# Kernel tuning notes

Hardware: AMD Instinct MI355X
Metric: run time of the kernel (lower is better)

The kernel has to match this reference:

```python
import jax, jax.numpy as jnp
import numpy as np

GAMMA = 0.9865
B, S, D = 8, 2048, 128


def setup_inputs() -> dict:
    key = jax.random.key(0)
    kq, kk, kv, kw = jax.random.split(key, 4)
    xq = jax.random.normal(kq, (B, S, D), dtype=jnp.float32)
    xk = jax.random.normal(kk, (B, S, D), dtype=jnp.float32)
    xv = jax.random.normal(kv, (B, S, D), dtype=jnp.float32)
    # NOTE: the original builds three Dense layers by repeating the SAME object,
    # so Q/K/V share a single no-bias weight matrix W.
    W = jax.random.normal(kw, (D, D), dtype=jnp.float32) * (1.0 / np.sqrt(D))
    return {"xq": xq, "xk": xk, "xv": xv, "W": W}


def _decay_matrix(seq_len, gamma):
    # Original: factors[i,j] = gamma^(i-j); keep upper triangle (j>=i); transpose.
    # Result: Dm[n,m] = gamma^(m-n) for n >= m, else 0 (lower triangular).
    n = jnp.arange(seq_len, dtype=jnp.float32)
    expo = n[None, :] - n[:, None]            # [S,S], entry (n,m) = m - n
    Dm = jnp.tril(jnp.float32(gamma) ** expo)  # zero out m > n before they'd matter
    return Dm


def reference(xq, xk, xv, W):
    Q = xq @ W
    K = xk @ W
    V = xv @ W
    d = Q.shape[-1]
    scores = jnp.einsum('bnd,bmd->bnm', Q, K) / jnp.sqrt(jnp.float32(d))
    Dm = _decay_matrix(Q.shape[1], GAMMA)
    # D /= reduce_sum(D, axis=1) ** 0.5  -> row-sums broadcast over LAST axis,
    # i.e. column m of D is divided by sqrt(rowsum[m]). Faithful to tf broadcasting.
    Dm = Dm / jnp.sqrt(jnp.sum(Dm, axis=1))
    scores = scores * Dm
    # per-batch norm: xs[n,m] / max(|sum_k xs[m,k]|, 1)  (tf broadcasting over last axis)
    s = jnp.sum(scores, axis=2)                       # [B,S]
    scores = scores / jnp.maximum(jnp.abs(s), 1.0)[:, None, :]
    return scores @ V
```

## Files before the change

kernel.cpp:

```cpp
#include <hip/hip_runtime.h>
#include <math.h>


constexpr int B = 8, S = 2048, D = 128;
constexpr int C = 64, NC = S / C;
constexpr int BS = B * S;
constexpr int NCH = B * NC;
#define GAMMA_F 0.9865f

typedef __attribute__((ext_vector_type(8))) short short8;
typedef __attribute__((ext_vector_type(8))) unsigned short ushort8;
typedef __attribute__((ext_vector_type(4))) float f32x4;

__device__ inline unsigned short f2bf(float f) {
  unsigned u = __builtin_bit_cast(unsigned, f);
  return (unsigned short)((u + 0x7FFF + ((u >> 16) & 1)) >> 16);
}
__device__ inline float bf2f(unsigned short h) {
  return __builtin_bit_cast(float, (unsigned)h << 16);
}

__global__ __launch_bounds__(128) void k_y(const float* __restrict__ xk,
                                           float* __restrict__ yc) {
  __shared__ float ksl[64];
  int bc = blockIdx.x, tid = threadIdx.x;
  float lgf = logf(GAMMA_F);
  if (tid < 64) {
    int n = (bc * 64 + tid) & (S - 1);
    float rs = (expf(-lgf * (float)(n + 1)) - 1.f) * (GAMMA_F / (1.f - GAMMA_F));
    ksl[tid] = expf(lgf * (float)n) / sqrtf(rs);
  }
  __syncthreads();
  const float* x = xk + (size_t)bc * 64 * 128 + tid;
  float a = 0.f;
#pragma unroll
  for (int j = 0; j < 64; j++) a = fmaf(ksl[j], x[j * 128], a);
  yc[(size_t)bc * 128 + tid] = a;
}

__global__ __launch_bounds__(512) void k_big(
    const float* __restrict__ xq, const float* __restrict__ xk,
    const float* __restrict__ xv, const float* __restrict__ W,
    const float* __restrict__ yc, unsigned short* __restrict__ qb,
    unsigned short* __restrict__ al, unsigned short* __restrict__ vbT,
    unsigned short* __restrict__ Hc) {
  __shared__ unsigned short qkv[3][64][136];
  __shared__ alignas(16) char ovl[36864];
  __shared__ float csp[128];
  __shared__ float ysum[128];
  __shared__ float cspp[4][128];
  __shared__ float invl[64];
  __shared__ float rsum_l[2][64];
  auto wt = (unsigned short(*)[136])ovl;
  auto kT = (unsigned short(*)[72])ovl;
  auto vT = (unsigned short(*)[72])(ovl + 18432);

  int bc = blockIdx.x, b = bc >> 5, c = bc & 31;
  int tid = threadIdx.x, w = tid >> 6, lane = tid & 63;
  int l15 = lane & 15, kg = (lane >> 4) * 8;
  float lgf = logf(GAMMA_F);

  for (int idx = tid; idx < 128 * 128; idx += 512) {
    int cc = idx >> 7, k = idx & 127;
    wt[cc][k] = f2bf(W[k * 128 + cc]);
  }
  if (tid < 128) {
    float a = 0.f;
    for (int cc = 0; cc < c; cc++) a += yc[(size_t)(b * NC + cc) * 128 + tid];
    ysum[tid] = a;
  }
  __syncthreads();

  int rt = w & 3, chh = w >> 2;
  {
    int arow = rt * 16 + l15;
    size_t grow = (size_t)(bc * 64 + arow) * 128;
    for (int mat = 0; mat < 3; mat++) {
      const float* X = (mat == 0) ? xq : ((mat == 1) ? xk : xv);
      f32x4 acc[4];
#pragma unroll
      for (int j = 0; j < 4; j++) acc[j] = (f32x4){0.f, 0.f, 0.f, 0.f};
#pragma unroll
      for (int t = 0; t < 4; t++) {
        int k0 = t * 32 + kg;
        const float* ap = X + grow + k0;
        float a8[8];
        *(f32x4*)(a8) = *(const f32x4*)ap;
        *(f32x4*)(a8 + 4) = *(const f32x4*)(ap + 4);
        short8 af;
#pragma unroll
        for (int i = 0; i < 8; i++) af[i] = (short)f2bf(a8[i]);
#pragma unroll
        for (int j = 0; j < 4; j++) {
          short8 bf = *(const short8*)&wt[(chh * 4 + j) * 16 + l15][k0];
          acc[j] = __builtin_amdgcn_mfma_f32_16x16x32_bf16(af, bf, acc[j], 0, 0, 0);
        }
      }
      int crow = rt * 16 + (lane >> 4) * 4;
#pragma unroll
      for (int rr = 0; rr < 4; rr++) {
        int row = crow + rr;
        int n = (bc * 64 + row) & (S - 1);
        float sc;
        if (mat == 0) {
          sc = expf(-lgf * (float)n) * 0.088388347f;
        } else if (mat == 1) {
          float rs = (expf(-lgf * (float)(n + 1)) - 1.f) * (GAMMA_F / (1.f - GAMMA_F));
          sc = expf(lgf * (float)n) / sqrtf(rs);
        } else {
          sc = 1.f;
        }
#pragma unroll
        for (int j = 0; j < 4; j++)
          qkv[mat][row][(chh * 4 + j) * 16 + l15] = f2bf(acc[j][rr] * sc);
      }
    }
  }
  {
    int d = tid & 127, q = tid >> 7;
    float part = 0.f;
#pragma unroll
    for (int k = 0; k < 32; k++) part = fmaf(ysum[32 * q + k], bf2f(wt[d][32 * q + k]), part);
    cspp[q][d] = part;
  }
  __syncthreads();

  if (tid < 128) csp[tid] = cspp[0][tid] + cspp[1][tid] + cspp[2][tid] + cspp[3][tid];
  {
    int row = tid >> 3, col = (tid & 7) * 16;
    unsigned short* dst = qb + (size_t)(bc * 64 + row) * 128 + col;
    *(ushort8*)dst = *(const ushort8*)&qkv[0][row][col];
    *(ushort8*)(dst + 8) = *(const ushort8*)&qkv[0][row][col + 8];
  }
  {
    int rt2 = w & 3, mh = w >> 2;
    int arow = rt2 * 16 + l15;
    int crow = rt2 * 16 + (lane >> 4) * 4;
    f32x4 a1[2];
#pragma unroll
    for (int mi = 0; mi < 2; mi++) a1[mi] = (f32x4){0.f, 0.f, 0.f, 0.f};
#pragma unroll
    for (int t = 0; t < 4; t++) {
      int k0 = t * 32 + kg;
      short8 af = *(const short8*)&qkv[0][arow][k0];
#pragma unroll
      for (int mi = 0; mi < 2; mi++) {
        short8 bf = *(const short8*)&qkv[1][(mh * 2 + mi) * 16 + l15][k0];
        a1[mi] = __builtin_amdgcn_mfma_f32_16x16x32_bf16(af, bf, a1[mi], 0, 0, 0);
      }
    }
    unsigned short* alg = al + (size_t)bc * 64 * 64;
    float rsp[4] = {0.f, 0.f, 0.f, 0.f};
#pragma unroll
    for (int mi = 0; mi < 2; mi++)
#pragma unroll
      for (int rr = 0; rr < 4; rr++) {
        int n_l = crow + rr, m_l = (mh * 2 + mi) * 16 + l15;
        float mv = (n_l >= m_l) ? a1[mi][rr] : 0.f;
        alg[n_l * 64 + m_l] = f2bf(mv);
        rsp[rr] += mv;
      }
#pragma unroll
    for (int rr = 0; rr < 4; rr++) {
      float r = rsp[rr];
      r += __shfl_xor(r, 1); r += __shfl_xor(r, 2);
      r += __shfl_xor(r, 4); r += __shfl_xor(r, 8);
      if (l15 == 0) rsum_l[mh][crow + rr] = r;
    }
  }
  {
    int d = tid & 127, mh2 = tid >> 7;
#pragma unroll
    for (int mg = 0; mg < 2; mg++) {
      ushort8 pk;
#pragma unroll
      for (int i = 0; i < 8; i++) pk[i] = qkv[1][mh2 * 16 + mg * 8 + i][d];
      *(ushort8*)&kT[d][mh2 * 16 + mg * 8] = pk;
    }
  }
  {
    int d = tid & 127, mh2 = tid >> 7;
#pragma unroll
    for (int mg = 0; mg < 2; mg++) {
      ushort8 pk;
#pragma unroll
      for (int i = 0; i < 8; i++) pk[i] = qkv[2][mh2 * 16 + mg * 8 + i][d];
      *(ushort8*)&vT[d][mh2 * 16 + mg * 8] = pk;
    }
  }
  __syncthreads();

  {
    int row = tid >> 3, part = tid & 7;
    ushort8 q8a = *(const ushort8*)&qkv[0][row][part * 16];
    ushort8 q8b = *(const ushort8*)&qkv[0][row][part * 16 + 8];
    float dot = 0.f;
#pragma unroll
    for (int ii = 0; ii < 8; ii++) {
      dot = fmaf(bf2f(q8a[ii]), csp[part * 16 + ii], dot);
      dot = fmaf(bf2f(q8b[ii]), csp[part * 16 + 8 + ii], dot);
    }
    dot += __shfl_xor(dot, 1); dot += __shfl_xor(dot, 2); dot += __shfl_xor(dot, 4);
    if (part == 0) {
      float s = rsum_l[0][row] + rsum_l[1][row] + dot;
      invl[row] = 1.f / fmaxf(fabsf(s), 1.f);
    }
  }
  __syncthreads();

  {
    int d = tid >> 2, ms = (tid & 3) * 16;
#pragma unroll
    for (int g = 0; g < 2; g++) {
      ushort8 v8 = *(const ushort8*)&vT[d][ms + g * 8];
      ushort8 o;
#pragma unroll
      for (int ii = 0; ii < 8; ii++) o[ii] = f2bf(bf2f(v8[ii]) * invl[ms + g * 8 + ii]);
      *(ushort8*)&vT[d][ms + g * 8] = o;
    }
  }
  __syncthreads();

  {
    f32x4 hacc[8];
#pragma unroll
    for (int j = 0; j < 8; j++) hacc[j] = (f32x4){0.f, 0.f, 0.f, 0.f};
#pragma unroll
    for (int t = 0; t < 2; t++) {
      int k0 = t * 32 + kg;
      short8 a2 = *(const short8*)&vT[w * 16 + l15][k0];
#pragma unroll
      for (int j = 0; j < 8; j++) {
        short8 bf = *(const short8*)&kT[j * 16 + l15][k0];
        hacc[j] = __builtin_amdgcn_mfma_f32_16x16x32_bf16(a2, bf, hacc[j], 0, 0, 0);
      }
    }
    unsigned short* g = Hc + (size_t)bc * D * D;
#pragma unroll
    for (int j = 0; j < 8; j++)
#pragma unroll
      for (int rr = 0; rr < 4; rr++)
        g[(size_t)(w * 16 + (lane >> 4) * 4 + rr) * D + j * 16 + l15] =
            f2bf(hacc[j][rr]);
  }
  {
    int d = tid >> 2, pp = (tid & 3) * 16;
    unsigned short* dst = vbT + (size_t)bc * D * C + (size_t)d * C + pp;
    *(ushort8*)(dst) = *(const ushort8*)&vT[d][pp];
    *(ushort8*)(dst + 8) = *(const ushort8*)&vT[d][pp + 8];
  }
}

__global__ __launch_bounds__(64) void k_gscan(const unsigned short* __restrict__ Hc,
                                              unsigned short* __restrict__ HS) {
  int b = blockIdx.x, gy = blockIdx.y, t = threadIdx.x;
  int d2 = gy * 4 + (t >> 4), d1 = (t & 15) * 8;
  size_t off = ((size_t)(b * NC) * D + d2) * D + d1;
  ushort8 v[NC];
#pragma unroll
  for (int c = 0; c < NC; c++)
    v[c] = *(const ushort8*)(Hc + off + (size_t)c * D * D);
  float run[8];
#pragma unroll
  for (int j = 0; j < 8; j++) run[j] = 0.f;
#pragma unroll
  for (int c = 0; c < NC; c++) {
    ushort8 o;
#pragma unroll
    for (int j = 0; j < 8; j++) {
      o[j] = f2bf(run[j]);
      run[j] += bf2f(v[c][j]);
    }
    *(ushort8*)(HS + off + (size_t)c * D * D) = o;
  }
}

__global__ __launch_bounds__(512) void k_out(
    const unsigned short* __restrict__ qb, const unsigned short* __restrict__ al,
    const unsigned short* __restrict__ vbT, const unsigned short* __restrict__ HS,
    float* __restrict__ out) {
  int bc = blockIdx.x, tid = threadIdx.x, w = tid >> 6, lane = tid & 63;
  int l15 = lane & 15;
  size_t base = (size_t)bc * C * D;
  int kg = (lane >> 4) * 8;
  int rt = w >> 1, ch = w & 1;
  int arow = rt * 16 + l15;
  int crow = rt * 16 + (lane >> 4) * 4;

  f32x4 acc[4];
#pragma unroll
  for (int j = 0; j < 4; j++) acc[j] = (f32x4){0.f, 0.f, 0.f, 0.f};
  const unsigned short* hrow = HS + (size_t)bc * D * D;
#pragma unroll
  for (int t = 0; t < 4; t++) {
    int k0 = t * 32 + kg;
    short8 af = *(const short8*)(qb + base + (size_t)arow * D + k0);
#pragma unroll
    for (int jj = 0; jj < 4; jj++) {
      int j = ch * 4 + jj;
      short8 bf = *(const short8*)(hrow + (size_t)(j * 16 + l15) * D + k0);
      acc[jj] = __builtin_amdgcn_mfma_f32_16x16x32_bf16(af, bf, acc[jj], 0, 0, 0);
    }
  }
  const unsigned short* alg = al + (size_t)bc * 64 * 64;
  const unsigned short* vt = vbT + (size_t)bc * D * C;
#pragma unroll
  for (int t = 0; t < 2; t++) {
    int k0 = t * 32 + kg;
    short8 af = *(const short8*)(alg + (size_t)arow * 64 + k0);
#pragma unroll
    for (int jj = 0; jj < 4; jj++) {
      int j = ch * 4 + jj;
      short8 bf = *(const short8*)(vt + (size_t)(j * 16 + l15) * C + k0);
      acc[jj] = __builtin_amdgcn_mfma_f32_16x16x32_bf16(af, bf, acc[jj], 0, 0, 0);
    }
  }
#pragma unroll
  for (int jj = 0; jj < 4; jj++)
#pragma unroll
    for (int rr = 0; rr < 4; rr++)
      out[base + (size_t)(crow + rr) * D + (ch * 4 + jj) * 16 + l15] = acc[jj][rr];
}

extern "C" void kernel_launch(void* const* d_in, const int* in_sizes, int n_in,
                              void* d_out, int out_size, void* d_ws, size_t ws_size,
                              hipStream_t stream) {
  const float* xq = (const float*)d_in[0];
  const float* xk = (const float*)d_in[1];
  const float* xv = (const float*)d_in[2];
  const float* W  = (const float*)d_in[3];
  float* out = (float*)d_out;

  char* p = (char*)d_ws;
  float* yc = (float*)p;                     p += (size_t)NCH * D * 4;
  unsigned short* qb  = (unsigned short*)p;  p += (size_t)BS * D * 2;
  unsigned short* al  = (unsigned short*)p;  p += (size_t)NCH * C * C * 2;
  unsigned short* vbT = (unsigned short*)p;  p += (size_t)NCH * D * C * 2;
  unsigned short* Hc  = (unsigned short*)p;  p += (size_t)NCH * D * D * 2;
  unsigned short* HS  = (unsigned short*)p;  p += (size_t)NCH * D * D * 2;

  hipLaunchKernelGGL(k_y, dim3(NCH), dim3(128), 0, stream, xk, yc);
  hipLaunchKernelGGL(k_big, dim3(NCH), dim3(512), 0, stream,
                     xq, xk, xv, W, yc, qb, al, vbT, Hc);
  hipLaunchKernelGGL(k_gscan, dim3(B, 32), dim3(64), 0, stream, Hc, HS);
  hipLaunchKernelGGL(k_out, dim3(NCH), dim3(512), 0, stream, qb, al, vbT, HS, out);
}
```

Baseline: 51.78 us.

## Fuse chunk-state prefix scan into output kernel and widen blocks to 1024 threads

Removes the separate k_gscan prefix-sum kernel and HS buffer. Each output block now sums the preceding chunks' Hc states itself into shared memory before the MFMA output step. k_big and the new output kernel are also redistributed to 1024 threads (16 waves), with work per wave halved. This saves a launch and a full HS write/read, but makes the per-block prefix sum redundant, so later chunks read up to 31 state matrices and the work is imbalanced across blocks.

```diff
diff --git a/kernel.cpp b/kernel.cpp
--- a/kernel.cpp
+++ b/kernel.cpp
@@ -38,7 +38,7 @@
   yc[(size_t)bc * 128 + tid] = a;
 }
 
-__global__ __launch_bounds__(512) void k_big(
+__global__ __launch_bounds__(1024, 1) void k_big(
     const float* __restrict__ xq, const float* __restrict__ xk,
     const float* __restrict__ xv, const float* __restrict__ W,
     const float* __restrict__ yc, unsigned short* __restrict__ qb,
@@ -48,9 +48,9 @@
   __shared__ alignas(16) char ovl[36864];
   __shared__ float csp[128];
   __shared__ float ysum[128];
-  __shared__ float cspp[4][128];
+  __shared__ float cspp[8][128];
   __shared__ float invl[64];
-  __shared__ float rsum_l[2][64];
+  __shared__ float rsum_l[4][64];
   auto wt = (unsigned short(*)[136])ovl;
   auto kT = (unsigned short(*)[72])ovl;
   auto vT = (unsigned short(*)[72])(ovl + 18432);
@@ -60,7 +60,7 @@
   int l15 = lane & 15, kg = (lane >> 4) * 8;
   float lgf = logf(GAMMA_F);
 
-  for (int idx = tid; idx < 128 * 128; idx += 512) {
+  for (int idx = tid; idx < 128 * 128; idx += 1024) {
     int cc = idx >> 7, k = idx & 127;
     wt[cc][k] = f2bf(W[k * 128 + cc]);
   }
@@ -71,15 +71,15 @@
   }
   __syncthreads();
 
-  int rt = w & 3, chh = w >> 2;
-  {
+  {
+    int rt = w & 3, cq = w >> 2;
     int arow = rt * 16 + l15;
     size_t grow = (size_t)(bc * 64 + arow) * 128;
     for (int mat = 0; mat < 3; mat++) {
       const float* X = (mat == 0) ? xq : ((mat == 1) ? xk : xv);
-      f32x4 acc[4];
-#pragma unroll
-      for (int j = 0; j < 4; j++) acc[j] = (f32x4){0.f, 0.f, 0.f, 0.f};
+      f32x4 acc[2];
+#pragma unroll
+      for (int j = 0; j < 2; j++) acc[j] = (f32x4){0.f, 0.f, 0.f, 0.f};
 #pragma unroll
       for (int t = 0; t < 4; t++) {
         int k0 = t * 32 + kg;
@@ -91,8 +91,8 @@
 #pragma unroll
         for (int i = 0; i < 8; i++) af[i] = (short)f2bf(a8[i]);
 #pragma unroll
-        for (int j = 0; j < 4; j++) {
-          short8 bf = *(const short8*)&wt[(chh * 4 + j) * 16 + l15][k0];
+        for (int j = 0; j < 2; j++) {
+          short8 bf = *(const short8*)&wt[(cq * 2 + j) * 16 + l15][k0];
           acc[j] = __builtin_amdgcn_mfma_f32_16x16x32_bf16(af, bf, acc[j], 0, 0, 0);
         }
       }
@@ -111,8 +111,8 @@
           sc = 1.f;
         }
 #pragma unroll
-        for (int j = 0; j < 4; j++)
-          qkv[mat][row][(chh * 4 + j) * 16 + l15] = f2bf(acc[j][rr] * sc);
+        for (int j = 0; j < 2; j++)
+          qkv[mat][row][(cq * 2 + j) * 16 + l15] = f2bf(acc[j][rr] * sc);
       }
     }
   }
@@ -120,185 +120,171 @@
     int d = tid & 127, q = tid >> 7;
     float part = 0.f;
 #pragma unroll
-    for (int k = 0; k < 32; k++) part = fmaf(ysum[32 * q + k], bf2f(wt[d][32 * q + k]), part);
+    for (int k = 0; k < 16; k++)
+      part = fmaf(ysum[16 * q + k], bf2f(wt[d][16 * q + k]), part);
     cspp[q][d] = part;
   }
   __syncthreads();
 
-  if (tid < 128) csp[tid] = cspp[0][tid] + cspp[1][tid] + cspp[2][tid] + cspp[3][tid];
-  {
-    int row = tid >> 3, col = (tid & 7) * 16;
-    unsigned short* dst = qb + (size_t)(bc * 64 + row) * 128 + col;
-    *(ushort8*)dst = *(const ushort8*)&qkv[0][row][col];
-    *(ushort8*)(dst + 8) = *(const ushort8*)&qkv[0][row][col + 8];
-  }
-  {
-    int rt2 = w & 3, mh = w >> 2;
+  if (tid < 128) {
+    float a = 0.f;
+#pragma unroll
+    for (int q = 0; q < 8; q++) a += cspp[q][tid];
+    csp[tid] = a;
+  }
+  {
+    int row = tid >> 4, col = (tid & 15) * 8;
+    *(ushort8*)(qb + (size_t)(bc * 64 + row) * 128 + col) =
+        *(const ushort8*)&qkv[0][row][col];
+  }
+  {
+    int rt2 = w & 3, mt = w >> 2;
     int arow = rt2 * 16 + l15;
     int crow = rt2 * 16 + (lane >> 4) * 4;
-    f32x4 a1[2];
-#pragma unroll
-    for (int mi = 0; mi < 2; mi++) a1[mi] = (f32x4){0.f, 0.f, 0.f, 0.f};
+    f32x4 a1 = (f32x4){0.f, 0.f, 0.f, 0.f};
 #pragma unroll
     for (int t = 0; t < 4; t++) {
       int k0 = t * 32 + kg;
       short8 af = *(const short8*)&qkv[0][arow][k0];
-#pragma unroll
-      for (int mi = 0; mi < 2; mi++) {
-        short8 bf = *(const short8*)&qkv[1][(mh * 2 + mi) * 16 + l15][k0];
-        a1[mi] = __builtin_amdgcn_mfma_f32_16x16x32_bf16(af, bf, a1[mi], 0, 0, 0);
-      }
+      short8 bf = *(const short8*)&qkv[1][mt * 16 + l15][k0];
+      a1 = __builtin_amdgcn_mfma_f32_16x16x32_bf16(af, bf, a1, 0, 0, 0);
     }
     unsigned short* alg = al + (size_t)bc * 64 * 64;
-    float rsp[4] = {0.f, 0.f, 0.f, 0.f};
-#pragma unroll
-    for (int mi = 0; mi < 2; mi++)
-#pragma unroll
-      for (int rr = 0; rr < 4; rr++) {
-        int n_l = crow + rr, m_l = (mh * 2 + mi) * 16 + l15;
-        float mv = (n_l >= m_l) ? a1[mi][rr] : 0.f;
-        alg[n_l * 64 + m_l] = f2bf(mv);
-        rsp[rr] += mv;
-      }
+    float rsp[4];
+#pragma unroll
+    for (int rr = 0; rr < 4; rr++) {
+      int n_l = crow + rr, m_l = mt * 16 + l15;
+      float mv = (n_l >= m_l) ? a1[rr] : 0.f;
+      alg[n_l * 64 + m_l] = f2bf(mv);
+      rsp[rr] = mv;
+    }
 #pragma unroll
     for (int rr = 0; rr < 4; rr++) {
       float r = rsp[rr];
       r += __shfl_xor(r, 1); r += __shfl_xor(r, 2);
       r += __shfl_xor(r, 4); r += __shfl_xor(r, 8);
-      if (l15 == 0) rsum_l[mh][crow + rr] = r;
-    }
-  }
-  {
-    int d = tid & 127, mh2 = tid >> 7;
-#pragma unroll
-    for (int mg = 0; mg < 2; mg++) {
-      ushort8 pk;
-#pragma unroll
-      for (int i = 0; i < 8; i++) pk[i] = qkv[1][mh2 * 16 + mg * 8 + i][d];
-      *(ushort8*)&kT[d][mh2 * 16 + mg * 8] = pk;
-    }
-  }
-  {
-    int d = tid & 127, mh2 = tid >> 7;
-#pragma unroll
-    for (int mg = 0; mg < 2; mg++) {
-      ushort8 pk;
-#pragma unroll
-      for (int i = 0; i < 8; i++) pk[i] = qkv[2][mh2 * 16 + mg * 8 + i][d];
-      *(ushort8*)&vT[d][mh2 * 16 + mg * 8] = pk;
-    }
-  }
-  __syncthreads();
-
-  {
-    int row = tid >> 3, part = tid & 7;
-    ushort8 q8a = *(const ushort8*)&qkv[0][row][part * 16];
-    ushort8 q8b = *(const ushort8*)&qkv[0][row][part * 16 + 8];
+      if (l15 == 0) rsum_l[mt][crow + rr] = r;
+    }
+  }
+  {
+    int d = tid & 127, g8 = tid >> 7;
+    ushort8 pk;
+#pragma unroll
+    for (int i = 0; i < 8; i++) pk[i] = qkv[1][g8 * 8 + i][d];
+    *(ushort8*)&kT[d][g8 * 8] = pk;
+  }
+  {
+    int d = tid & 127, g8 = tid >> 7;
+    ushort8 pk;
+#pragma unroll
+    for (int i = 0; i < 8; i++) pk[i] = qkv[2][g8 * 8 + i][d];
+    *(ushort8*)&vT[d][g8 * 8] = pk;
+  }
+  __syncthreads();
+
+  {
+    int row = tid >> 4, part = tid & 15;
+    ushort8 q8 = *(const ushort8*)&qkv[0][row][part * 8];
     float dot = 0.f;
 #pragma unroll
-    for (int ii = 0; ii < 8; ii++) {
-      dot = fmaf(bf2f(q8a[ii]), csp[part * 16 + ii], dot);
-      dot = fmaf(bf2f(q8b[ii]), csp[part * 16 + 8 + ii], dot);
-    }
-    dot += __shfl_xor(dot, 1); dot += __shfl_xor(dot, 2); dot += __shfl_xor(dot, 4);
+    for (int ii = 0; ii < 8; ii++) dot = fmaf(bf2f(q8[ii]), csp[part * 8 + ii], dot);
+    dot += __shfl_xor(dot, 1); dot += __shfl_xor(dot, 2);
+    dot += __shfl_xor(dot, 4); dot += __shfl_xor(dot, 8);
     if (part == 0) {
-      float s = rsum_l[0][row] + rsum_l[1][row] + dot;
+      float s = rsum_l[0][row] + rsum_l[1][row] + rsum_l[2][row] + rsum_l[3][row] + dot;
       invl[row] = 1.f / fmaxf(fabsf(s), 1.f);
     }
   }
   __syncthreads();
 
   {
-    int d = tid >> 2, ms = (tid & 3) * 16;
-#pragma unroll
-    for (int g = 0; g < 2; g++) {
-      ushort8 v8 = *(const ushort8*)&vT[d][ms + g * 8];
-      ushort8 o;
-#pragma unroll
-      for (int ii = 0; ii < 8; ii++) o[ii] = f2bf(bf2f(v8[ii]) * invl[ms + g * 8 + ii]);
-      *(ushort8*)&vT[d][ms + g * 8] = o;
-    }
-  }
-  __syncthreads();
-
-  {
-    f32x4 hacc[8];
-#pragma unroll
-    for (int j = 0; j < 8; j++) hacc[j] = (f32x4){0.f, 0.f, 0.f, 0.f};
+    int d = tid >> 3, ms = (tid & 7) * 8;
+    ushort8 v8 = *(const ushort8*)&vT[d][ms];
+    ushort8 o;
+#pragma unroll
+    for (int ii = 0; ii < 8; ii++) o[ii] = f2bf(bf2f(v8[ii]) * invl[ms + ii]);
+    *(ushort8*)&vT[d][ms] = o;
+  }
+  __syncthreads();
+
+  {
+    int d2t = w >> 1, jh = w & 1;
+    f32x4 hacc[4];
+#pragma unroll
+    for (int j = 0; j < 4; j++) hacc[j] = (f32x4){0.f, 0.f, 0.f, 0.f};
 #pragma unroll
     for (int t = 0; t < 2; t++) {
       int k0 = t * 32 + kg;
-      short8 a2 = *(const short8*)&vT[w * 16 + l15][k0];
-#pragma unroll
-      for (int j = 0; j < 8; j++) {
-        short8 bf = *(const short8*)&kT[j * 16 + l15][k0];
+      short8 a2 = *(const short8*)&vT[d2t * 16 + l15][k0];
+#pragma unroll
+      for (int j = 0; j < 4; j++) {
+        short8 bf = *(const short8*)&kT[(jh * 4 + j) * 16 + l15][k0];
         hacc[j] = __builtin_amdgcn_mfma_f32_16x16x32_bf16(a2, bf, hacc[j], 0, 0, 0);
       }
     }
     unsigned short* g = Hc + (size_t)bc * D * D;
 #pragma unroll
-    for (int j = 0; j < 8; j++)
+    for (int j = 0; j < 4; j++)
 #pragma unroll
       for (int rr = 0; rr < 4; rr++)
-        g[(size_t)(w * 16 + (lane >> 4) * 4 + rr) * D + j * 16 + l15] =
+        g[(size_t)(d2t * 16 + (lane >> 4) * 4 + rr) * D + (jh * 4 + j) * 16 + l15] =
             f2bf(hacc[j][rr]);
   }
   {
-    int d = tid >> 2, pp = (tid & 3) * 16;
-    unsigned short* dst = vbT + (size_t)bc * D * C + (size_t)d * C + pp;
-    *(ushort8*)(dst) = *(const ushort8*)&vT[d][pp];
-    *(ushort8*)(dst + 8) = *(const ushort8*)&vT[d][pp + 8];
-  }
-}
-
-__global__ __launch_bounds__(64) void k_gscan(const unsigned short* __restrict__ Hc,
-                                              unsigned short* __restrict__ HS) {
-  int b = blockIdx.x, gy = blockIdx.y, t = threadIdx.x;
-  int d2 = gy * 4 + (t >> 4), d1 = (t & 15) * 8;
-  size_t off = ((size_t)(b * NC) * D + d2) * D + d1;
-  ushort8 v[NC];
-#pragma unroll
-  for (int c = 0; c < NC; c++)
-    v[c] = *(const ushort8*)(Hc + off + (size_t)c * D * D);
-  float run[8];
-#pragma unroll
-  for (int j = 0; j < 8; j++) run[j] = 0.f;
-#pragma unroll
-  for (int c = 0; c < NC; c++) {
-    ushort8 o;
-#pragma unroll
-    for (int j = 0; j < 8; j++) {
-      o[j] = f2bf(run[j]);
-      run[j] += bf2f(v[c][j]);
-    }
-    *(ushort8*)(HS + off + (size_t)c * D * D) = o;
-  }
-}
-
-__global__ __launch_bounds__(512) void k_out(
+    int d = tid >> 3, pp = (tid & 7) * 8;
+    *(ushort8*)(vbT + (size_t)bc * D * C + (size_t)d * C + pp) =
+        *(const ushort8*)&vT[d][pp];
+  }
+}
+
+__global__ __launch_bounds__(1024, 1) void k_out2(
     const unsigned short* __restrict__ qb, const unsigned short* __restrict__ al,
-    const unsigned short* __restrict__ vbT, const unsigned short* __restrict__ HS,
+    const unsigned short* __restrict__ vbT, const unsigned short* __restrict__ Hc,
     float* __restrict__ out) {
-  int bc = blockIdx.x, tid = threadIdx.x, w = tid >> 6, lane = tid & 63;
-  int l15 = lane & 15;
+  __shared__ unsigned short SEL[128][136];
+  int bc = blockIdx.x, b = bc >> 5, c = bc & 31;
+  int tid = threadIdx.x, w = tid >> 6, lane = tid & 63;
+  int l15 = lane & 15, kg = (lane >> 4) * 8;
+
+  {
+    int slot = tid * 16;
+    int r = slot >> 7, col = slot & 127;
+    float accf[16];
+#pragma unroll
+    for (int i = 0; i < 16; i++) accf[i] = 0.f;
+    const unsigned short* base = Hc + (size_t)(b * NC) * D * D + (size_t)r * D + col;
+    for (int cc = 0; cc < c; cc++) {
+      ushort8 v0 = *(const ushort8*)(base + (size_t)cc * D * D);
+      ushort8 v1 = *(const ushort8*)(base + (size_t)cc * D * D + 8);
+#pragma unroll
+      for (int i = 0; i < 8; i++) {
+        accf[i] += bf2f(v0[i]);
+        accf[8 + i] += bf2f(v1[i]);
+      }
+    }
+    ushort8 o0, o1;
+#pragma unroll
+    for (int i = 0; i < 8; i++) { o0[i] = f2bf(accf[i]); o1[i] = f2bf(accf[8 + i]); }
+    *(ushort8*)&SEL[r][col] = o0;
+    *(ushort8*)&SEL[r][col + 8] = o1;
+  }
+  __syncthreads();
+
   size_t base = (size_t)bc * C * D;
-  int kg = (lane >> 4) * 8;
-  int rt = w >> 1, ch = w & 1;
+  int rt = w & 3, ch = w >> 2;
   int arow = rt * 16 + l15;
   int crow = rt * 16 + (lane >> 4) * 4;
 
-  f32x4 acc[4];
-#pragma unroll
-  for (int j = 0; j < 4; j++) acc[j] = (f32x4){0.f, 0.f, 0.f, 0.f};
-  const unsigned short* hrow = HS + (size_t)bc * D * D;
+  f32x4 acc[2];
+#pragma unroll
+  for (int j = 0; j < 2; j++) acc[j] = (f32x4){0.f, 0.f, 0.f, 0.f};
 #pragma unroll
   for (int t = 0; t < 4; t++) {
     int k0 = t * 32 + kg;
     short8 af = *(const short8*)(qb + base + (size_t)arow * D + k0);
 #pragma unroll
-    for (int jj = 0; jj < 4; jj++) {
-      int j = ch * 4 + jj;
-      short8 bf = *(const short8*)(hrow + (size_t)(j * 16 + l15) * D + k0);
+    for (int jj = 0; jj < 2; jj++) {
+      short8 bf = *(const short8*)&SEL[(ch * 2 + jj) * 16 + l15][k0];
       acc[jj] = __builtin_amdgcn_mfma_f32_16x16x32_bf16(af, bf, acc[jj], 0, 0, 0);
     }
   }
@@ -309,17 +295,16 @@
     int k0 = t * 32 + kg;
     short8 af = *(const short8*)(alg + (size_t)arow * 64 + k0);
 #pragma unroll
-    for (int jj = 0; jj < 4; jj++) {
-      int j = ch * 4 + jj;
-      short8 bf = *(const short8*)(vt + (size_t)(j * 16 + l15) * C + k0);
+    for (int jj = 0; jj < 2; jj++) {
+      short8 bf = *(const short8*)(vt + (size_t)((ch * 2 + jj) * 16 + l15) * C + k0);
       acc[jj] = __builtin_amdgcn_mfma_f32_16x16x32_bf16(af, bf, acc[jj], 0, 0, 0);
     }
   }
 #pragma unroll
-  for (int jj = 0; jj < 4; jj++)
+  for (int jj = 0; jj < 2; jj++)
 #pragma unroll
     for (int rr = 0; rr < 4; rr++)
-      out[base + (size_t)(crow + rr) * D + (ch * 4 + jj) * 16 + l15] = acc[jj][rr];
+      out[base + (size_t)(crow + rr) * D + (ch * 2 + jj) * 16 + l15] = acc[jj][rr];
 }
 
 extern "C" void kernel_launch(void* const* d_in, const int* in_sizes, int n_in,
@@ -337,11 +322,9 @@
   unsigned short* al  = (unsigned short*)p;  p += (size_t)NCH * C * C * 2;
   unsigned short* vbT = (unsigned short*)p;  p += (size_t)NCH * D * C * 2;
   unsigned short* Hc  = (unsigned short*)p;  p += (size_t)NCH * D * D * 2;
-  unsigned short* HS  = (unsigned short*)p;  p += (size_t)NCH * D * D * 2;
 
   hipLaunchKernelGGL(k_y, dim3(NCH), dim3(128), 0, stream, xk, yc);
-  hipLaunchKernelGGL(k_big, dim3(NCH), dim3(512), 0, stream,
+  hipLaunchKernelGGL(k_big, dim3(NCH), dim3(1024), 0, stream,
                      xq, xk, xv, W, yc, qb, al, vbT, Hc);
-  hipLaunchKernelGGL(k_gscan, dim3(B, 32), dim3(64), 0, stream, Hc, HS);
-  hipLaunchKernelGGL(k_out, dim3(NCH), dim3(512), 0, stream, qb, al, vbT, HS, out);
-}
+  hipLaunchKernelGGL(k_out2, dim3(NCH), dim3(1024), 0, stream, qb, al, vbT, Hc, out);
+}
```

After: 61.10 us. +18.0%, slower.

## Parallelize chunk scan across four groups and split output columns over blocks

Applied to the files above, without the earlier changes.

The state prefix scan over the 32 chunks now runs as a two-level scan. Four wavefronts each sum 8 chunks, exchange their totals through shared memory, and then scan locally. This replaces a single 64-thread block that walked all 32 chunks serially. The output kernel doubles its grid by splitting the 128 output columns across two blocks, so more blocks run in parallel but the A operand (q rows and the alpha tile) is loaded twice.

```diff
diff --git a/kernel.cpp b/kernel.cpp
--- a/kernel.cpp
+++ b/kernel.cpp
@@ -251,27 +251,42 @@
   }
 }
 
-__global__ __launch_bounds__(64) void k_gscan(const unsigned short* __restrict__ Hc,
-                                              unsigned short* __restrict__ HS) {
-  int b = blockIdx.x, gy = blockIdx.y, t = threadIdx.x;
-  int d2 = gy * 4 + (t >> 4), d1 = (t & 15) * 8;
+__global__ __launch_bounds__(256) void k_gscan(const unsigned short* __restrict__ Hc,
+                                               unsigned short* __restrict__ HS) {
+  __shared__ float ttot[4][64][8];
+  int b = blockIdx.x, gy = blockIdx.y;
+  int tid = threadIdx.x, g = tid >> 6, slot = tid & 63;
+  int d2 = gy * 4 + (slot >> 4), d1 = (slot & 15) * 8;
   size_t off = ((size_t)(b * NC) * D + d2) * D + d1;
-  ushort8 v[NC];
-#pragma unroll
-  for (int c = 0; c < NC; c++)
-    v[c] = *(const ushort8*)(Hc + off + (size_t)c * D * D);
+  ushort8 v[8];
+  float tot[8];
+#pragma unroll
+  for (int j = 0; j < 8; j++) tot[j] = 0.f;
+#pragma unroll
+  for (int i = 0; i < 8; i++) {
+    v[i] = *(const ushort8*)(Hc + off + (size_t)(g * 8 + i) * D * D);
+#pragma unroll
+    for (int j = 0; j < 8; j++) tot[j] += bf2f(v[i][j]);
+  }
+#pragma unroll
+  for (int j = 0; j < 8; j++) ttot[g][slot][j] = tot[j];
+  __syncthreads();
   float run[8];
 #pragma unroll
   for (int j = 0; j < 8; j++) run[j] = 0.f;
-#pragma unroll
-  for (int c = 0; c < NC; c++) {
+  for (int gg = 0; gg < 4; gg++)
+    if (gg < g)
+#pragma unroll
+      for (int j = 0; j < 8; j++) run[j] += ttot[gg][slot][j];
+#pragma unroll
+  for (int i = 0; i < 8; i++) {
     ushort8 o;
 #pragma unroll
     for (int j = 0; j < 8; j++) {
       o[j] = f2bf(run[j]);
-      run[j] += bf2f(v[c][j]);
-    }
-    *(ushort8*)(HS + off + (size_t)c * D * D) = o;
+      run[j] += bf2f(v[i][j]);
+    }
+    *(ushort8*)(HS + off + (size_t)(g * 8 + i) * D * D) = o;
   }
 }
 
@@ -279,25 +294,26 @@
     const unsigned short* __restrict__ qb, const unsigned short* __restrict__ al,
     const unsigned short* __restrict__ vbT, const unsigned short* __restrict__ HS,
     float* __restrict__ out) {
-  int bc = blockIdx.x, tid = threadIdx.x, w = tid >> 6, lane = tid & 63;
+  int bc = blockIdx.x, ch2 = blockIdx.y;
+  int tid = threadIdx.x, w = tid >> 6, lane = tid & 63;
   int l15 = lane & 15;
   size_t base = (size_t)bc * C * D;
   int kg = (lane >> 4) * 8;
-  int rt = w >> 1, ch = w & 1;
+  int rt = w >> 1, chw = w & 1;
   int arow = rt * 16 + l15;
   int crow = rt * 16 + (lane >> 4) * 4;
 
-  f32x4 acc[4];
-#pragma unroll
-  for (int j = 0; j < 4; j++) acc[j] = (f32x4){0.f, 0.f, 0.f, 0.f};
+  f32x4 acc[2];
+#pragma unroll
+  for (int j = 0; j < 2; j++) acc[j] = (f32x4){0.f, 0.f, 0.f, 0.f};
   const unsigned short* hrow = HS + (size_t)bc * D * D;
 #pragma unroll
   for (int t = 0; t < 4; t++) {
     int k0 = t * 32 + kg;
     short8 af = *(const short8*)(qb + base + (size_t)arow * D + k0);
 #pragma unroll
-    for (int jj = 0; jj < 4; jj++) {
-      int j = ch * 4 + jj;
+    for (int jj = 0; jj < 2; jj++) {
+      int j = ch2 * 4 + chw * 2 + jj;
       short8 bf = *(const short8*)(hrow + (size_t)(j * 16 + l15) * D + k0);
       acc[jj] = __builtin_amdgcn_mfma_f32_16x16x32_bf16(af, bf, acc[jj], 0, 0, 0);
     }
@@ -309,17 +325,18 @@
     int k0 = t * 32 + kg;
     short8 af = *(const short8*)(alg + (size_t)arow * 64 + k0);
 #pragma unroll
-    for (int jj = 0; jj < 4; jj++) {
-      int j = ch * 4 + jj;
+    for (int jj = 0; jj < 2; jj++) {
+      int j = ch2 * 4 + chw * 2 + jj;
       short8 bf = *(const short8*)(vt + (size_t)(j * 16 + l15) * C + k0);
       acc[jj] = __builtin_amdgcn_mfma_f32_16x16x32_bf16(af, bf, acc[jj], 0, 0, 0);
     }
   }
 #pragma unroll
-  for (int jj = 0; jj < 4; jj++)
+  for (int jj = 0; jj < 2; jj++)
 #pragma unroll
     for (int rr = 0; rr < 4; rr++)
-      out[base + (size_t)(crow + rr) * D + (ch * 4 + jj) * 16 + l15] = acc[jj][rr];
+      out[base + (size_t)(crow + rr) * D + (ch2 * 4 + chw * 2 + jj) * 16 + l15] =
+          acc[jj][rr];
 }
 
 extern "C" void kernel_launch(void* const* d_in, const int* in_sizes, int n_in,
@@ -342,6 +359,6 @@
   hipLaunchKernelGGL(k_y, dim3(NCH), dim3(128), 0, stream, xk, yc);
   hipLaunchKernelGGL(k_big, dim3(NCH), dim3(512), 0, stream,
                      xq, xk, xv, W, yc, qb, al, vbT, Hc);
-  hipLaunchKernelGGL(k_gscan, dim3(B, 32), dim3(64), 0, stream, Hc, HS);
-  hipLaunchKernelGGL(k_out, dim3(NCH), dim3(512), 0, stream, qb, al, vbT, HS, out);
-}
+  hipLaunchKernelGGL(k_gscan, dim3(B, 32), dim3(256), 0, stream, Hc, HS);
+  hipLaunchKernelGGL(k_out, dim3(NCH, 2), dim3(512), 0, stream, qb, al, vbT, HS, out);
+}
```

Measured after the change: 52.42 us. About the same (+1.2%).
